# Kernel optimization log

Measured on AMD Instinct MI355X. Metric: run time of the kernel, lower is better.

The kernel has to match this reference:

```python
import jax, jax.numpy as jnp
import numpy as np

EMB = 1024
HEADS = 16
HEAD_DIM = EMB // HEADS
DFF = 4 * EMB
EPS = 1e-5


def gelu_tanh(x):
    c = jnp.sqrt(jnp.asarray(2.0 / jnp.pi, dtype=x.dtype))
    return 0.5 * x * (1.0 + jnp.tanh(c * (x + 0.044715 * x ** 3)))


def layernorm(x, scale, shift):
    mean = jnp.mean(x, axis=-1, keepdims=True)
    var = jnp.mean((x - mean) ** 2, axis=-1, keepdims=True)
    return scale * ((x - mean) / jnp.sqrt(var + EPS)) + shift


def setup_inputs() -> dict:
    key = jax.random.key(0)
    ks = jax.random.split(key, 12)
    s = 0.02
    return {
        "x": jax.random.normal(ks[0], (2, 2048, EMB), dtype=jnp.float32),
        "Wq": jax.random.normal(ks[1], (EMB, EMB), dtype=jnp.float32) * s,
        "Wk": jax.random.normal(ks[2], (EMB, EMB), dtype=jnp.float32) * s,
        "Wv": jax.random.normal(ks[3], (EMB, EMB), dtype=jnp.float32) * s,
        "Wo": jax.random.normal(ks[4], (EMB, EMB), dtype=jnp.float32) * s,
        "bo": jnp.zeros((EMB,), dtype=jnp.float32),
        "W1": jax.random.normal(ks[5], (EMB, DFF), dtype=jnp.float32) * s,
        "b1": jnp.zeros((DFF,), dtype=jnp.float32),
        "W2": jax.random.normal(ks[6], (DFF, EMB), dtype=jnp.float32) * s,
        "b2": jnp.zeros((EMB,), dtype=jnp.float32),
        "g1": jnp.ones((EMB,), dtype=jnp.float32),
        "s1": jnp.zeros((EMB,), dtype=jnp.float32),
        "g2": jnp.ones((EMB,), dtype=jnp.float32),
        "s2": jnp.zeros((EMB,), dtype=jnp.float32),
    }


def reference(x, Wq, Wk, Wv, Wo, bo, W1, b1, W2, b2, g1, s1, g2, s2):
    B, S, E = x.shape
    # attention sub-block (pre-norm, residual)
    h = layernorm(x, g1, s1)
    Q = (h @ Wq).reshape(B, S, HEADS, HEAD_DIM)
    K = (h @ Wk).reshape(B, S, HEADS, HEAD_DIM)
    V = (h @ Wv).reshape(B, S, HEADS, HEAD_DIM)
    # scores: [B, H, S, S]
    scores = jnp.einsum("bqhd,bkhd->bhqk", Q, K)
    causal = jnp.tril(jnp.ones((S, S), dtype=bool))
    scores = jnp.where(causal, scores, -jnp.inf)
    attn = jax.nn.softmax(scores / np.sqrt(HEAD_DIM), axis=-1)
    ctx = jnp.einsum("bhqk,bkhd->bqhd", attn, V).reshape(B, S, E)
    x = x + (ctx @ Wo + bo)
    # FFN sub-block
    h = layernorm(x, g2, s2)
    h = gelu_tanh(h @ W1 + b1) @ W2 + b2
    return x + h
```

## Files before the change

kernel.cpp:

```cpp
#include <hip/hip_runtime.h>
#include <hip/hip_bf16.h>

typedef __attribute__((ext_vector_type(8))) short short8;
typedef __attribute__((ext_vector_type(4))) float f32x4;

#define EMB   1024
#define DFF   4096
#define S_LEN 2048
#define NB    2
#define MTOT  (NB * S_LEN)
#define HEADS 16
#define HDIM  64
#define QKN   2048

__device__ __forceinline__ float bf2f(unsigned short u) {
  return __uint_as_float(((unsigned int)u) << 16);
}
__device__ __forceinline__ unsigned short f2bf(float f) {
  unsigned int x = __float_as_uint(f);
  unsigned int r = (x + 0x7fffu + ((x >> 16) & 1u)) >> 16;
  return (unsigned short)r;
}
__device__ __forceinline__ unsigned int cvtpk(float a, float b) {
  unsigned int r;
  asm("v_cvt_pk_bf16_f32 %0, %1, %2" : "=v"(r) : "v"(a), "v"(b));
  return r;
}

__device__ __forceinline__ void gl_lds16(const unsigned short* g, unsigned short* l) {
  __builtin_amdgcn_global_load_lds(
      (const __attribute__((address_space(1))) unsigned int*)g,
      (__attribute__((address_space(3))) unsigned int*)l, 16, 0, 0);
}

__device__ __forceinline__ float gelu_tanh_f(float v) {
  float u = v + 0.044715f * v * v * v;
  float t = tanhf(0.7978845608028654f * u);
  return 0.5f * v * (1.0f + t);
}

__global__ __launch_bounds__(256) void prep_kernel(
    const float* __restrict__ Wq, const float* __restrict__ Wk,
    const float* __restrict__ Wv, const float* __restrict__ Wo,
    const float* __restrict__ W1, const float* __restrict__ W2,
    unsigned short* __restrict__ wtQ, unsigned short* __restrict__ wtK,
    unsigned short* __restrict__ wtV, unsigned short* __restrict__ wtO,
    unsigned short* __restrict__ wtW1, unsigned short* __restrict__ wtW2,
    const float* __restrict__ X, const float* __restrict__ g1,
    const float* __restrict__ s1, unsigned short* __restrict__ H)
{
  const int bid = (int)blockIdx.x;
  const int tid = threadIdx.x;

  if (bid >= 6144) {
    const int row = bid - 6144;
    const float* xr = X + (size_t)row * EMB;
    float4 v = *(const float4*)(xr + tid * 4);
    float s  = v.x + v.y + v.z + v.w;
    float ss = v.x * v.x + v.y * v.y + v.z * v.z + v.w * v.w;
#pragma unroll
    for (int off = 32; off > 0; off >>= 1) {
      s  += __shfl_xor(s, off);
      ss += __shfl_xor(ss, off);
    }
    __shared__ float rs[4], rss[4];
    const int wid = tid >> 6;
    if ((tid & 63) == 0) { rs[wid] = s; rss[wid] = ss; }
    __syncthreads();
    s  = rs[0] + rs[1] + rs[2] + rs[3];
    ss = rss[0] + rss[1] + rss[2] + rss[3];
    const float mean = s * (1.f / EMB);
    const float var  = ss * (1.f / EMB) - mean * mean;
    const float rstd = rsqrtf(var + 1e-5f);
    float4 gv = *(const float4*)(g1 + tid * 4);
    float4 sv = *(const float4*)(s1 + tid * 4);
    ushort4 o;
    o.x = f2bf((v.x - mean) * rstd * gv.x + sv.x);
    o.y = f2bf((v.y - mean) * rstd * gv.y + sv.y);
    o.z = f2bf((v.z - mean) * rstd * gv.z + sv.z);
    o.w = f2bf((v.w - mean) * rstd * gv.w + sv.w);
    *(ushort4*)(H + (size_t)row * EMB + tid * 4) = o;
    return;
  }

  __shared__ float t[64][33];
  const int tx = tid & 31, ty = tid >> 5;
  const float* W; unsigned short* Wt; int K, N, local;
  if (bid < 2048) {
    const int sel = bid >> 9; local = bid & 511; K = 1024; N = 1024;
    W  = sel == 0 ? Wq  : sel == 1 ? Wk  : sel == 2 ? Wv  : Wo;
    Wt = sel == 0 ? wtQ : sel == 1 ? wtK : sel == 2 ? wtV : wtO;
  } else if (bid < 4096) {
    local = bid - 2048; K = 1024; N = 4096; W = W1; Wt = wtW1;
  } else {
    local = bid - 4096; K = 4096; N = 1024; W = W2; Wt = wtW2;
  }
  const int nbx = N >> 5;
  const int n0 = (local % nbx) * 32, k0 = (local / nbx) * 64;
#pragma unroll
  for (int i = 0; i < 8; ++i) {
    const int kr = i * 8 + ty;
    t[kr][tx] = W[(size_t)(k0 + kr) * N + n0 + tx];
  }
  __syncthreads();
#pragma unroll
  for (int i = 0; i < 4; ++i) {
    const int r = ty + i * 8;
    const unsigned int u = cvtpk(t[2 * tx][r], t[2 * tx + 1][r]);
    *(unsigned int*)(&Wt[(size_t)(n0 + r) * K + k0 + 2 * tx]) = u;
  }
}

__global__ __launch_bounds__(256) void ln_kernel(
    const float* __restrict__ X, const float* __restrict__ g,
    const float* __restrict__ sh, unsigned short* __restrict__ H)
{
  const int row = blockIdx.x, t = threadIdx.x;
  const float* xr = X + (size_t)row * EMB;
  float4 v = *(const float4*)(xr + t * 4);
  float s  = v.x + v.y + v.z + v.w;
  float ss = v.x * v.x + v.y * v.y + v.z * v.z + v.w * v.w;
#pragma unroll
  for (int off = 32; off > 0; off >>= 1) {
    s  += __shfl_xor(s, off);
    ss += __shfl_xor(ss, off);
  }
  __shared__ float rs[4], rss[4];
  const int wid = t >> 6;
  if ((t & 63) == 0) { rs[wid] = s; rss[wid] = ss; }
  __syncthreads();
  s  = rs[0] + rs[1] + rs[2] + rs[3];
  ss = rss[0] + rss[1] + rss[2] + rss[3];
  const float mean = s * (1.f / EMB);
  const float var  = ss * (1.f / EMB) - mean * mean;
  const float rstd = rsqrtf(var + 1e-5f);
  float4 gv = *(const float4*)(g + t * 4);
  float4 sv = *(const float4*)(sh + t * 4);
  ushort4 o;
  o.x = f2bf((v.x - mean) * rstd * gv.x + sv.x);
  o.y = f2bf((v.y - mean) * rstd * gv.y + sv.y);
  o.z = f2bf((v.z - mean) * rstd * gv.z + sv.z);
  o.w = f2bf((v.w - mean) * rstd * gv.w + sv.w);
  *(ushort4*)(H + (size_t)row * EMB + t * 4) = o;
}

__global__ __launch_bounds__(512, 2) void gemm8p(
    const unsigned short* __restrict__ A, const unsigned short* __restrict__ Bt,
    const float* __restrict__ bias, unsigned short* __restrict__ outb)
{
  __shared__ unsigned short As[2][256 * 64];
  __shared__ unsigned short Bs[2][256 * 64];

  const int tid = threadIdx.x;
  const int lane = tid & 63, wid = tid >> 6;
  const int bid = (int)blockIdx.x;
  const int swz = (bid & 7) * 32 + (bid >> 3);
  const int by = swz >> 4, bx = swz & 15;
  const int m0 = by * 256, n0 = bx * 256;
  const int wr = wid >> 2, wc = wid & 3;
  const int l16 = lane & 15, kg = lane >> 4;

  const int sr  = lane >> 3;
  const int scs = ((lane & 7) ^ (lane >> 3)) * 8;
  const int rx  = l16 & 7;

  const unsigned short* Ab = A + (size_t)m0 * 1024;
  const unsigned short* Bb = Bt + (size_t)n0 * 1024;

  f32x4 acc[8][4];
#pragma unroll
  for (int i = 0; i < 8; ++i)
#pragma unroll
    for (int j = 0; j < 4; ++j) acc[i][j] = (f32x4){0.f, 0.f, 0.f, 0.f};

#define STGH(ldsdst, gb, grow0, kt_)                                           \
  do {                                                                         \
    _Pragma("unroll")                                                          \
    for (int i_ = 0; i_ < 2; ++i_) {                                           \
      const int c_ = wid * 2 + i_;                                             \
      gl_lds16((gb) + (size_t)((grow0) + c_ * 8 + sr) * 1024 + (kt_) * 64 + scs, \
               (ldsdst) + c_ * 512);                                           \
    }                                                                          \
  } while (0)

#define PHASE(mp, STAGE_STMT, TAIL_STMT)                                       \
  do {                                                                         \
    short8 af[2][2];                                                           \
    _Pragma("unroll")                                                          \
    for (int i = 0; i < 2; ++i)                                                \
      _Pragma("unroll")                                                        \
      for (int kk = 0; kk < 2; ++kk)                                           \
        af[i][kk] = *(const short8*)(                                          \
            &As[b][(wr * 128 + ((mp) * 2 + i) * 16 + l16) * 64 +               \
                   ((kg + kk * 4) ^ rx) * 8]);                                 \
    STAGE_STMT;                                                                \
    __builtin_amdgcn_s_barrier();                                              \
    asm volatile("s_waitcnt lgkmcnt(0)" ::: "memory");                         \
    __builtin_amdgcn_s_setprio(1);                                             \
    _Pragma("unroll")                                                          \
    for (int kk = 0; kk < 2; ++kk)                                             \
      _Pragma("unroll")                                                        \
      for (int j = 0; j < 4; ++j)                                              \
        _Pragma("unroll")                                                      \
        for (int i = 0; i < 2; ++i)                                            \
          acc[(mp) * 2 + i][j] = __builtin_amdgcn_mfma_f32_16x16x32_bf16(      \
              af[i][kk], bf[j][kk], acc[(mp) * 2 + i][j], 0, 0, 0);            \
    __builtin_amdgcn_s_setprio(0);                                             \
    TAIL_STMT;                                                                 \
    __builtin_amdgcn_s_barrier();                                              \
  } while (0)

  STGH(&As[0][0], Ab, 0, 0);   STGH(&As[0][128 * 64], Ab, 128, 0);
  STGH(&Bs[0][0], Bb, 0, 0);   STGH(&Bs[0][128 * 64], Bb, 128, 0);
  STGH(&As[1][0], Ab, 0, 1);   STGH(&As[1][128 * 64], Ab, 128, 1);
  STGH(&Bs[1][0], Bb, 0, 1);   STGH(&Bs[1][128 * 64], Bb, 128, 1);
  asm volatile("s_waitcnt vmcnt(8)" ::: "memory");
  __builtin_amdgcn_s_barrier();

  const int nt = 16;
  for (int t = 0; t < nt; ++t) {
    const int b = t & 1;
    short8 bf[4][2];
#pragma unroll
    for (int j = 0; j < 4; ++j)
#pragma unroll
      for (int kk = 0; kk < 2; ++kk)
        bf[j][kk] = *(const short8*)(
            &Bs[b][(wc * 64 + j * 16 + l16) * 64 + ((kg + kk * 4) ^ rx) * 8]);

    PHASE(0, if (t >= 1 && t + 1 < nt) STGH(&As[b ^ 1][0], Ab, 0, t + 1), );
    PHASE(1, if (t >= 1 && t + 1 < nt) STGH(&As[b ^ 1][128 * 64], Ab, 128, t + 1), );
    PHASE(2, if (t + 2 < nt) STGH(&Bs[b][0], Bb, 0, t + 2), );
    PHASE(3, if (t + 2 < nt) STGH(&Bs[b][128 * 64], Bb, 128, t + 2),
          if (t + 2 < nt) { asm volatile("s_waitcnt vmcnt(4)" ::: "memory"); }
          else            { asm volatile("s_waitcnt vmcnt(0)" ::: "memory"); });
  }
#undef PHASE
#undef STGH

#pragma unroll
  for (int i = 0; i < 8; ++i) {
#pragma unroll
    for (int j = 0; j < 4; ++j) {
      const int c = n0 + wc * 64 + j * 16 + l16;
      const float bc = bias[c];
#pragma unroll
      for (int r = 0; r < 4; ++r) {
        const int row = m0 + wr * 128 + i * 16 + kg * 4 + r;
        outb[(size_t)row * 4096 + c] = f2bf(gelu_tanh_f(acc[i][j][r] + bc));
      }
    }
  }
}

template <int MODE, int BN, int BKT, int NBUF>
__global__ __launch_bounds__(256, 2) void gemm_gl(
    const unsigned short* __restrict__ A, const unsigned short* __restrict__ Bt,
    int M, int N, int Kloop, int Kld, int nbx,
    const float* __restrict__ bias, const float* __restrict__ resf,
    float* __restrict__ outf, unsigned short* __restrict__ outb,
    unsigned short* __restrict__ vt)
{
  constexpr int NFRAG = BN / 32;
  constexpr int KK    = BKT / 32;
  constexpr int ACH   = 128 * BKT / 512;
  constexpr int BCH   = BN  * BKT / 512;
  __shared__ unsigned short As[NBUF][128 * BKT];
  __shared__ unsigned short Bs[NBUF][BN * BKT];

  const int tid = threadIdx.x;
  const int lane = tid & 63, wid = tid >> 6;
  const int nwg = (int)gridDim.x;
  const int cpx = nwg >> 3;
  const int bid = (int)blockIdx.x;
  const int swz = (bid & 7) * cpx + (bid >> 3);
  const int by = swz / nbx;
  const int bx = swz - by * nbx;
  const int m0 = by * 128, n0 = bx * BN;
  const int wr = wid >> 1, wc = wid & 1;
  const int l16 = lane & 15, kg = lane >> 4;

  int sr, scs;
  if constexpr (BKT == 32) {
    sr  = lane >> 2;
    scs = ((lane & 3) ^ ((lane >> 3) & 3)) * 8;
  } else {
    sr  = lane >> 3;
    scs = ((lane & 7) ^ (lane >> 3)) * 8;
  }
  const int rx = (BKT == 32) ? ((l16 >> 1) & 3) : (l16 & 7);

  const unsigned short* Abase = A + (size_t)m0 * Kld;
  const unsigned short* Bbase = Bt + (size_t)n0 * Kld;

  f32x4 acc[4][NFRAG];
#pragma unroll
  for (int i = 0; i < 4; ++i)
#pragma unroll
    for (int j = 0; j < NFRAG; ++j) acc[i][j] = (f32x4){0.f, 0.f, 0.f, 0.f};

  const int nt = Kloop / BKT;
  constexpr int RPC = (BKT == 32) ? 16 : 8;

#define STAGE(buf, t)                                                          \
  do {                                                                         \
    const int k0_ = (t) * BKT;                                                 \
    _Pragma("unroll")                                                          \
    for (int i_ = 0; i_ < ACH / 4; ++i_) {                                     \
      const int chunk_ = wid * (ACH / 4) + i_;                                 \
      gl_lds16(Abase + (size_t)(chunk_ * RPC + sr) * Kld + k0_ + scs,          \
               &As[buf][0] + chunk_ * 512);                                    \
    }                                                                          \
    _Pragma("unroll")                                                          \
    for (int i_ = 0; i_ < BCH / 4; ++i_) {                                     \
      const int chunk_ = wid * (BCH / 4) + i_;                                 \
      gl_lds16(Bbase + (size_t)(chunk_ * RPC + sr) * Kld + k0_ + scs,          \
               &Bs[buf][0] + chunk_ * 512);                                    \
    }                                                                          \
  } while (0)

#define VM_WAIT()                                                              \
  do {                                                                         \
    constexpr int W_ = ((ACH + BCH) / 4) * (NBUF - 1);                         \
    if constexpr (W_ == 3)      asm volatile("s_waitcnt vmcnt(3)" ::: "memory"); \
    else if constexpr (W_ == 4) asm volatile("s_waitcnt vmcnt(4)" ::: "memory"); \
    else if constexpr (W_ == 6) asm volatile("s_waitcnt vmcnt(6)" ::: "memory"); \
    else if constexpr (W_ == 8) asm volatile("s_waitcnt vmcnt(8)" ::: "memory"); \
    else                        asm volatile("s_waitcnt vmcnt(12)" ::: "memory"); \
  } while (0)

  STAGE(0, 0);
  STAGE(1, 1);
  if constexpr (NBUF == 3) STAGE(2, 2);
  VM_WAIT();
  __builtin_amdgcn_s_barrier();

  int b = 0;
  for (int t = 0; t < nt; ++t) {
    short8 af[4][KK], bfr[NFRAG][KK];
#pragma unroll
    for (int i = 0; i < 4; ++i)
#pragma unroll
      for (int kk = 0; kk < KK; ++kk)
        af[i][kk] = *(const short8*)(
            &As[b][(wr * 64 + i * 16 + l16) * BKT + ((kg + kk * 4) ^ rx) * 8]);
#pragma unroll
    for (int j = 0; j < NFRAG; ++j)
#pragma unroll
      for (int kk = 0; kk < KK; ++kk)
        bfr[j][kk] = *(const short8*)(
            &Bs[b][(wc * (BN / 2) + j * 16 + l16) * BKT + ((kg + kk * 4) ^ rx) * 8]);
#pragma unroll
    for (int kk = 0; kk < KK; ++kk)
#pragma unroll
      for (int i = 0; i < 4; ++i)
#pragma unroll
        for (int j = 0; j < NFRAG; ++j)
          acc[i][j] = __builtin_amdgcn_mfma_f32_16x16x32_bf16(af[i][kk], bfr[j][kk], acc[i][j], 0, 0, 0);
    asm volatile("s_waitcnt lgkmcnt(0)" ::: "memory");
    __builtin_amdgcn_s_barrier();
    if (t + NBUF < nt) {
      STAGE(b, t + NBUF);
      VM_WAIT();
    } else {
      asm volatile("s_waitcnt vmcnt(0)" ::: "memory");
    }
    __builtin_amdgcn_s_barrier();
    if constexpr (NBUF == 2) b ^= 1;
    else                     b = (b == 2) ? 0 : b + 1;
  }
#undef STAGE
#undef VM_WAIT

#pragma unroll
  for (int i = 0; i < 4; ++i) {
#pragma unroll
    for (int j = 0; j < NFRAG; ++j) {
      const int c = n0 + wc * (BN / 2) + j * 16 + l16;
      if constexpr (MODE == 0) {
        if (c >= 2048) {
          const int row0 = m0 + wr * 64 + i * 16 + kg * 4;
          const int dcol = c - 2048;
          ushort4 w4;
          w4.x = f2bf(acc[i][j][0]); w4.y = f2bf(acc[i][j][1]);
          w4.z = f2bf(acc[i][j][2]); w4.w = f2bf(acc[i][j][3]);
          *(ushort4*)(&vt[((size_t)((row0 >> 11) * 16 + (dcol >> 6)) * 64 +
                           (dcol & 63)) * 2048 + (row0 & 2047)]) = w4;
        } else {
          const float sc = (c < 1024) ? 0.18033688011112042f : 1.0f;
#pragma unroll
          for (int r = 0; r < 4; ++r) {
            const int row = m0 + wr * 64 + i * 16 + kg * 4 + r;
            outb[(size_t)row * QKN + c] = f2bf(acc[i][j][r] * sc);
          }
        }
      } else {
#pragma unroll
        for (int r = 0; r < 4; ++r) {
          const int row = m0 + wr * 64 + i * 16 + kg * 4 + r;
          const size_t idx = (size_t)row * N + c;
          float v = acc[i][j][r];
          if constexpr (MODE == 1) {
            outf[idx] = v + bias[c] + resf[idx];
          } else if constexpr (MODE == 2) {
            outb[idx] = f2bf(gelu_tanh_f(v + bias[c]));
          } else {
            outf[idx] = v + bias[c] + resf[idx];
          }
        }
      }
    }
  }
}

__global__ __launch_bounds__(256) void attn_mfma(
    const unsigned short* __restrict__ qkv, const unsigned short* __restrict__ Vt,
    unsigned short* __restrict__ ctx)
{
  __shared__ unsigned short Ks[128][64];
  __shared__ unsigned short Vs[64][128];
  __shared__ unsigned short Ps[4][2][16][128];

  const int tid  = threadIdx.x;
  const int lane = tid & 63, wv = tid >> 6;
  const int l16  = lane & 15, kg = lane >> 4;
  const int bid  = (int)blockIdx.x;
  const int swz  = (bid & 7) * 64 + (bid >> 3);
  const int pair = swz & 15;
  const int bh   = swz >> 4;
  const int b    = bh >> 4, h = bh & 15;
  const int qtg0 = pair;
  const int qtg1 = 31 - pair;

  const size_t qbase  = ((size_t)b * S_LEN) * QKN + h * HDIM;
  const size_t kbase  = qbase + 1024;
  const size_t vtbase = ((size_t)bh * HDIM) * S_LEN;
  const size_t cbase  = ((size_t)b * S_LEN) * EMB + h * HDIM;

  short8 qf[2][2];
#pragma unroll
  for (int g = 0; g < 2; ++g) {
    const int qt = g ? qtg1 : qtg0;
    const unsigned short* qrow =
        qkv + qbase + (size_t)(qt * 64 + wv * 16 + l16) * QKN;
    qf[g][0] = *(const short8*)(qrow + kg * 8);
    qf[g][1] = *(const short8*)(qrow + 32 + kg * 8);
  }

  f32x4 o[2][4];
#pragma unroll
  for (int g = 0; g < 2; ++g)
#pragma unroll
    for (int dt = 0; dt < 4; ++dt) o[g][dt] = (f32x4){0.f, 0.f, 0.f, 0.f};
  float m[2] = {-1e30f, -1e30f}, l[2] = {0.f, 0.f};

  const int kr2 = tid >> 1, kh = tid & 1;
  const int ksx = kr2 & 7;
  const int vr = tid >> 2, vc = tid & 3;
  const int vsx = vr & 7;
  const int rx = l16 & 7;

  const int nkt = (qtg1 + 2) >> 1;

  const unsigned short* ksrc = qkv + kbase + (size_t)kr2 * QKN + kh * 32;
  const unsigned short* vsrc = Vt + vtbase + (size_t)vr * S_LEN + vc * 32;
  short8 kv0 = *(const short8*)(ksrc);
  short8 kv1 = *(const short8*)(ksrc + 8);
  short8 kv2 = *(const short8*)(ksrc + 16);
  short8 kv3 = *(const short8*)(ksrc + 24);
  short8 vv0 = *(const short8*)(vsrc);
  short8 vv1 = *(const short8*)(vsrc + 8);
  short8 vv2 = *(const short8*)(vsrc + 16);
  short8 vv3 = *(const short8*)(vsrc + 24);

  for (int kt = 0; kt < nkt; ++kt) {
    __syncthreads();
    *(short8*)(&Ks[kr2][((kh * 4 + 0) ^ ksx) * 8]) = kv0;
    *(short8*)(&Ks[kr2][((kh * 4 + 1) ^ ksx) * 8]) = kv1;
    *(short8*)(&Ks[kr2][((kh * 4 + 2) ^ ksx) * 8]) = kv2;
    *(short8*)(&Ks[kr2][((kh * 4 + 3) ^ ksx) * 8]) = kv3;
    *(short8*)(&Vs[vr][((vc * 4 + 0) ^ vsx) * 8]) = vv0;
    *(short8*)(&Vs[vr][((vc * 4 + 1) ^ vsx) * 8]) = vv1;
    *(short8*)(&Vs[vr][((vc * 4 + 2) ^ vsx) * 8]) = vv2;
    *(short8*)(&Vs[vr][((vc * 4 + 3) ^ vsx) * 8]) = vv3;
    __syncthreads();

    if (kt + 1 < nkt) {
      const unsigned short* kn =
          qkv + kbase + (size_t)((kt + 1) * 128 + kr2) * QKN + kh * 32;
      const unsigned short* vn =
          Vt + vtbase + (size_t)vr * S_LEN + (kt + 1) * 128 + vc * 32;
      kv0 = *(const short8*)(kn);
      kv1 = *(const short8*)(kn + 8);
      kv2 = *(const short8*)(kn + 16);
      kv3 = *(const short8*)(kn + 24);
      vv0 = *(const short8*)(vn);
      vv1 = *(const short8*)(vn + 8);
      vv2 = *(const short8*)(vn + 16);
      vv3 = *(const short8*)(vn + 24);
    }

    const bool act0 = (2 * kt <= qtg0);

    float fac[2] = {1.f, 1.f};
    bool resc[2] = {false, false};
#pragma unroll
    for (int g = 0; g < 2; ++g) {
      if (g == 0 && !act0) continue;
      const int qt = g ? qtg1 : qtg0;

      f32x4 sa[8];
      __builtin_amdgcn_s_setprio(1);
#pragma unroll
      for (int j = 0; j < 8; ++j) {
        short8 kf0 = *(const short8*)(&Ks[j * 16 + l16][(kg ^ rx) * 8]);
        short8 kf1 = *(const short8*)(&Ks[j * 16 + l16][((kg + 4) ^ rx) * 8]);
        sa[j] = (f32x4){0.f, 0.f, 0.f, 0.f};
        sa[j] = __builtin_amdgcn_mfma_f32_16x16x32_bf16(kf0, qf[g][0], sa[j], 0, 0, 0);
        sa[j] = __builtin_amdgcn_mfma_f32_16x16x32_bf16(kf1, qf[g][1], sa[j], 0, 0, 0);
      }
      __builtin_amdgcn_s_setprio(0);

      const int qloc = qt * 64 + wv * 16 + l16;
      if (kt * 128 + 127 > qt * 64 + wv * 16) {
#pragma unroll
        for (int j = 0; j < 8; ++j)
#pragma unroll
          for (int r = 0; r < 4; ++r)
            if (kt * 128 + j * 16 + kg * 4 + r > qloc) sa[j][r] = -1e30f;
      }

      float mx = fmaxf(fmaxf(sa[0][0], sa[0][1]), fmaxf(sa[0][2], sa[0][3]));
#pragma unroll
      for (int j = 1; j < 8; ++j) {
        float mj = fmaxf(fmaxf(sa[j][0], sa[j][1]), fmaxf(sa[j][2], sa[j][3]));
        mx = fmaxf(mx, mj);
      }
      mx = fmaxf(mx, __shfl_xor(mx, 16));
      mx = fmaxf(mx, __shfl_xor(mx, 32));
      if (!__all(mx - m[g] <= 8.0f)) {
        const float mn = fmaxf(m[g], mx);
        fac[g] = exp2f(m[g] - mn);
        m[g] = mn;
        resc[g] = true;
      }
      const float mcur = m[g];
      float ps = 0.f;
#pragma unroll
      for (int j = 0; j < 8; ++j) {
        float p0 = exp2f(sa[j][0] - mcur);
        float p1 = exp2f(sa[j][1] - mcur);
        float p2 = exp2f(sa[j][2] - mcur);
        float p3 = exp2f(sa[j][3] - mcur);
        sa[j][0] = p0; sa[j][1] = p1; sa[j][2] = p2; sa[j][3] = p3;
        ps += (p0 + p1) + (p2 + p3);
      }
      ps += __shfl_xor(ps, 16);
      ps += __shfl_xor(ps, 32);
      l[g] = l[g] * fac[g] + ps;

#pragma unroll
      for (int j = 0; j < 8; ++j) {
        uint2 pw;
        pw.x = cvtpk(sa[j][0], sa[j][1]);
        pw.y = cvtpk(sa[j][2], sa[j][3]);
        *(uint2*)(&Ps[wv][g][l16][((2 * j + (kg >> 1)) ^ rx) * 8 + (kg & 1) * 4]) = pw;
      }
    }

#pragma unroll
    for (int g = 0; g < 2; ++g) {
      if (resc[g]) {
#pragma unroll
        for (int dt = 0; dt < 4; ++dt)
#pragma unroll
          for (int r = 0; r < 4; ++r) o[g][dt][r] *= fac[g];
      }
    }

    short8 pf[2][4];
#pragma unroll
    for (int g = 0; g < 2; ++g) {
      if (g == 0 && !act0) continue;
#pragma unroll
      for (int s = 0; s < 4; ++s)
        pf[g][s] = *(const short8*)(&Ps[wv][g][l16][((4 * s + kg) ^ rx) * 8]);
    }
    __builtin_amdgcn_s_setprio(1);
#pragma unroll
    for (int dt = 0; dt < 4; ++dt) {
#pragma unroll
      for (int s = 0; s < 4; ++s) {
        short8 vf = *(const short8*)(&Vs[dt * 16 + l16][((4 * s + kg) ^ rx) * 8]);
#pragma unroll
        for (int g = 0; g < 2; ++g) {
          if (g == 0 && !act0) continue;
          o[g][dt] = __builtin_amdgcn_mfma_f32_16x16x32_bf16(vf, pf[g][s], o[g][dt], 0, 0, 0);
        }
      }
    }
    __builtin_amdgcn_s_setprio(0);
  }

#pragma unroll
  for (int g = 0; g < 2; ++g) {
    const int qt = g ? qtg1 : qtg0;
    const float inv = 1.0f / l[g];
    const int qrow = qt * 64 + wv * 16 + l16;
#pragma unroll
    for (int dt = 0; dt < 4; ++dt) {
      uint2 cw;
      cw.x = cvtpk(o[g][dt][0] * inv, o[g][dt][1] * inv);
      cw.y = cvtpk(o[g][dt][2] * inv, o[g][dt][3] * inv);
      *(uint2*)(&ctx[cbase + (size_t)qrow * EMB + dt * 16 + kg * 4]) = cw;
    }
  }
}

extern "C" void kernel_launch(void* const* d_in, const int* in_sizes, int n_in,
                              void* d_out, int out_size, void* d_ws, size_t ws_size,
                              hipStream_t stream)
{
  const float* x  = (const float*)d_in[0];
  const float* Wq = (const float*)d_in[1];
  const float* Wk = (const float*)d_in[2];
  const float* Wv = (const float*)d_in[3];
  const float* Wo = (const float*)d_in[4];
  const float* bo = (const float*)d_in[5];
  const float* W1 = (const float*)d_in[6];
  const float* b1 = (const float*)d_in[7];
  const float* W2 = (const float*)d_in[8];
  const float* b2 = (const float*)d_in[9];
  const float* g1 = (const float*)d_in[10];
  const float* s1 = (const float*)d_in[11];
  const float* g2 = (const float*)d_in[12];
  const float* s2 = (const float*)d_in[13];

  float* out = (float*)d_out;
  char* ws = (char*)d_ws;
  const size_t MB = 1024 * 1024;
  unsigned short* wtQ  = (unsigned short*)(ws + 0 * MB);
  unsigned short* wtK  = (unsigned short*)(ws + 2 * MB);
  unsigned short* wtV  = (unsigned short*)(ws + 4 * MB);
  unsigned short* wtO  = (unsigned short*)(ws + 6 * MB);
  unsigned short* wtW1 = (unsigned short*)(ws + 8 * MB);
  unsigned short* wtW2 = (unsigned short*)(ws + 16 * MB);
  unsigned short* h    = (unsigned short*)(ws + 24 * MB);
  unsigned short* qkv  = (unsigned short*)(ws + 32 * MB);
  unsigned short* Vt   = (unsigned short*)(ws + 56 * MB);
  unsigned short* ctxb = h;
  unsigned short* h2   = h;
  unsigned short* gbuf = qkv;

  prep_kernel<<<dim3(10240), 256, 0, stream>>>(
      Wq, Wk, Wv, Wo, W1, W2, wtQ, wtK, wtV, wtO, wtW1, wtW2, x, g1, s1, h);

  gemm_gl<0, 128, 32, 2><<<dim3(24 * 32), 256, 0, stream>>>(
      h, wtQ, MTOT, 3072, 1024, 1024, 24, nullptr, nullptr, nullptr, qkv, Vt);

  attn_mfma<<<dim3(512), 256, 0, stream>>>(qkv, Vt, ctxb);

  gemm_gl<1, 64, 64, 2><<<dim3(16 * 32), 256, 0, stream>>>(
      ctxb, wtO, MTOT, 1024, 1024, 1024, 16, bo, x, out, nullptr, nullptr);

  ln_kernel<<<MTOT, 256, 0, stream>>>(out, g2, s2, h2);

  gemm8p<<<dim3(256), 512, 0, stream>>>(h2, wtW1, b1, gbuf);

  gemm_gl<3, 64, 64, 2><<<dim3(16 * 32), 256, 0, stream>>>(
      gbuf, wtW2, MTOT, 1024, DFF, DFF, 16, b2, out, out, nullptr, nullptr);
}
```

Measured before the change: 233.1 us.

## Skip fully masked causal sub-tiles and process query groups sequentially in attention

Inside the attention kernel, each 16-key sub-tile that lies entirely above the causal diagonal for a wave's 16 query rows is now skipped. That removes its QK MFMAs, masking, exp and PV MFMAs, and its P entries are written as zero. The PV product is moved into the per-group loop, so the P buffer in shared memory shrinks to one group per wave and the V fragments are reloaded for each group instead of shared across both. This cuts wasted work on diagonal tiles and LDS usage, but it adds branches and more LDS reads of V, and it serializes the two groups' phases.

```diff
diff --git a/kernel.cpp b/kernel.cpp
--- a/kernel.cpp
+++ b/kernel.cpp
@@ -419,7 +419,7 @@
 {
   __shared__ unsigned short Ks[128][64];
   __shared__ unsigned short Vs[64][128];
-  __shared__ unsigned short Ps[4][2][16][128];
+  __shared__ unsigned short Ps[4][16][128];
 
   const int tid  = threadIdx.x;
   const int lane = tid & 63, wv = tid >> 6;
@@ -501,105 +501,103 @@
     }
 
     const bool act0 = (2 * kt <= qtg0);
-
-    float fac[2] = {1.f, 1.f};
-    bool resc[2] = {false, false};
+    const int kb = kt * 128;
+
 #pragma unroll
     for (int g = 0; g < 2; ++g) {
       if (g == 0 && !act0) continue;
       const int qt = g ? qtg1 : qtg0;
+      const int qwmax = qt * 64 + wv * 16 + 15;
 
       f32x4 sa[8];
       __builtin_amdgcn_s_setprio(1);
 #pragma unroll
       for (int j = 0; j < 8; ++j) {
-        short8 kf0 = *(const short8*)(&Ks[j * 16 + l16][(kg ^ rx) * 8]);
-        short8 kf1 = *(const short8*)(&Ks[j * 16 + l16][((kg + 4) ^ rx) * 8]);
-        sa[j] = (f32x4){0.f, 0.f, 0.f, 0.f};
-        sa[j] = __builtin_amdgcn_mfma_f32_16x16x32_bf16(kf0, qf[g][0], sa[j], 0, 0, 0);
-        sa[j] = __builtin_amdgcn_mfma_f32_16x16x32_bf16(kf1, qf[g][1], sa[j], 0, 0, 0);
+        if (kb + j * 16 <= qwmax) {
+          short8 kf0 = *(const short8*)(&Ks[j * 16 + l16][(kg ^ rx) * 8]);
+          short8 kf1 = *(const short8*)(&Ks[j * 16 + l16][((kg + 4) ^ rx) * 8]);
+          sa[j] = (f32x4){0.f, 0.f, 0.f, 0.f};
+          sa[j] = __builtin_amdgcn_mfma_f32_16x16x32_bf16(kf0, qf[g][0], sa[j], 0, 0, 0);
+          sa[j] = __builtin_amdgcn_mfma_f32_16x16x32_bf16(kf1, qf[g][1], sa[j], 0, 0, 0);
+        }
       }
       __builtin_amdgcn_s_setprio(0);
 
       const int qloc = qt * 64 + wv * 16 + l16;
-      if (kt * 128 + 127 > qt * 64 + wv * 16) {
+      if (kb + 127 > qt * 64 + wv * 16) {
 #pragma unroll
         for (int j = 0; j < 8; ++j)
-#pragma unroll
-          for (int r = 0; r < 4; ++r)
-            if (kt * 128 + j * 16 + kg * 4 + r > qloc) sa[j][r] = -1e30f;
-      }
-
-      float mx = fmaxf(fmaxf(sa[0][0], sa[0][1]), fmaxf(sa[0][2], sa[0][3]));
-#pragma unroll
-      for (int j = 1; j < 8; ++j) {
-        float mj = fmaxf(fmaxf(sa[j][0], sa[j][1]), fmaxf(sa[j][2], sa[j][3]));
-        mx = fmaxf(mx, mj);
-      }
+          if (kb + j * 16 <= qwmax)
+#pragma unroll
+            for (int r = 0; r < 4; ++r)
+              if (kb + j * 16 + kg * 4 + r > qloc) sa[j][r] = -1e30f;
+      }
+
+      float mx = -1e30f;
+#pragma unroll
+      for (int j = 0; j < 8; ++j)
+        if (kb + j * 16 <= qwmax)
+          mx = fmaxf(mx, fmaxf(fmaxf(sa[j][0], sa[j][1]), fmaxf(sa[j][2], sa[j][3])));
       mx = fmaxf(mx, __shfl_xor(mx, 16));
       mx = fmaxf(mx, __shfl_xor(mx, 32));
+      float fac = 1.f;
+      bool resc = false;
       if (!__all(mx - m[g] <= 8.0f)) {
         const float mn = fmaxf(m[g], mx);
-        fac[g] = exp2f(m[g] - mn);
+        fac = exp2f(m[g] - mn);
         m[g] = mn;
-        resc[g] = true;
+        resc = true;
       }
       const float mcur = m[g];
       float ps = 0.f;
 #pragma unroll
       for (int j = 0; j < 8; ++j) {
-        float p0 = exp2f(sa[j][0] - mcur);
-        float p1 = exp2f(sa[j][1] - mcur);
-        float p2 = exp2f(sa[j][2] - mcur);
-        float p3 = exp2f(sa[j][3] - mcur);
-        sa[j][0] = p0; sa[j][1] = p1; sa[j][2] = p2; sa[j][3] = p3;
-        ps += (p0 + p1) + (p2 + p3);
+        if (kb + j * 16 <= qwmax) {
+          float p0 = exp2f(sa[j][0] - mcur);
+          float p1 = exp2f(sa[j][1] - mcur);
+          float p2 = exp2f(sa[j][2] - mcur);
+          float p3 = exp2f(sa[j][3] - mcur);
+          sa[j][0] = p0; sa[j][1] = p1; sa[j][2] = p2; sa[j][3] = p3;
+          ps += (p0 + p1) + (p2 + p3);
+        }
       }
       ps += __shfl_xor(ps, 16);
       ps += __shfl_xor(ps, 32);
-      l[g] = l[g] * fac[g] + ps;
+      l[g] = l[g] * fac + ps;
 
 #pragma unroll
       for (int j = 0; j < 8; ++j) {
         uint2 pw;
-        pw.x = cvtpk(sa[j][0], sa[j][1]);
-        pw.y = cvtpk(sa[j][2], sa[j][3]);
-        *(uint2*)(&Ps[wv][g][l16][((2 * j + (kg >> 1)) ^ rx) * 8 + (kg & 1) * 4]) = pw;
-      }
+        if (kb + j * 16 <= qwmax) {
+          pw.x = cvtpk(sa[j][0], sa[j][1]);
+          pw.y = cvtpk(sa[j][2], sa[j][3]);
+        } else {
+          pw.x = 0u; pw.y = 0u;
+        }
+        *(uint2*)(&Ps[wv][l16][((2 * j + (kg >> 1)) ^ rx) * 8 + (kg & 1) * 4]) = pw;
+      }
+
+      if (resc) {
+#pragma unroll
+        for (int dt = 0; dt < 4; ++dt)
+#pragma unroll
+          for (int r = 0; r < 4; ++r) o[g][dt][r] *= fac;
+      }
+
+      __builtin_amdgcn_s_setprio(1);
+#pragma unroll
+      for (int s = 0; s < 4; ++s) {
+        if (kb + s * 32 <= qwmax) {
+          short8 pfv = *(const short8*)(&Ps[wv][l16][((4 * s + kg) ^ rx) * 8]);
+#pragma unroll
+          for (int dt = 0; dt < 4; ++dt) {
+            short8 vf = *(const short8*)(&Vs[dt * 16 + l16][((4 * s + kg) ^ rx) * 8]);
+            o[g][dt] = __builtin_amdgcn_mfma_f32_16x16x32_bf16(vf, pfv, o[g][dt], 0, 0, 0);
+          }
+        }
+      }
+      __builtin_amdgcn_s_setprio(0);
     }
-
-#pragma unroll
-    for (int g = 0; g < 2; ++g) {
-      if (resc[g]) {
-#pragma unroll
-        for (int dt = 0; dt < 4; ++dt)
-#pragma unroll
-          for (int r = 0; r < 4; ++r) o[g][dt][r] *= fac[g];
-      }
-    }
-
-    short8 pf[2][4];
-#pragma unroll
-    for (int g = 0; g < 2; ++g) {
-      if (g == 0 && !act0) continue;
-#pragma unroll
-      for (int s = 0; s < 4; ++s)
-        pf[g][s] = *(const short8*)(&Ps[wv][g][l16][((4 * s + kg) ^ rx) * 8]);
-    }
-    __builtin_amdgcn_s_setprio(1);
-#pragma unroll
-    for (int dt = 0; dt < 4; ++dt) {
-#pragma unroll
-      for (int s = 0; s < 4; ++s) {
-        short8 vf = *(const short8*)(&Vs[dt * 16 + l16][((4 * s + kg) ^ rx) * 8]);
-#pragma unroll
-        for (int g = 0; g < 2; ++g) {
-          if (g == 0 && !act0) continue;
-          o[g][dt] = __builtin_amdgcn_mfma_f32_16x16x32_bf16(vf, pf[g][s], o[g][dt], 0, 0, 0);
-        }
-      }
-    }
-    __builtin_amdgcn_s_setprio(0);
   }
 
 #pragma unroll
```

After: 238.2 us. +2.2%, slower.
